# Kernel tuning notes

Hardware: AMD Instinct MI355X
Metric: run time of the kernel (lower is better)

## Reference

```python
import jax, jax.numpy as jnp
import numpy as np

EMB = 768
EPS = 1e-5

def setup_inputs() -> dict:
    key = jax.random.key(0)
    ks = jax.random.split(key, 7)
    B, S, D = 8, 2048, EMB
    s = 1.0 / np.sqrt(D)
    return {
        "h_": jax.random.normal(ks[0], (B, S, D), dtype=jnp.float32),
        "ln_gamma": jnp.ones((D,), jnp.float32),
        "ln_beta": jnp.zeros((D,), jnp.float32),
        "wq": jax.random.normal(ks[1], (D, D), jnp.float32) * s,
        "bq": jax.random.normal(ks[2], (D,), jnp.float32) * 0.01,
        "wk": jax.random.normal(ks[3], (D, D), jnp.float32) * s,
        "bk": jax.random.normal(ks[4], (D,), jnp.float32) * 0.01,
    }

def reference(h_, ln_gamma, ln_beta, wq, bq, wk, bk):
    # LayerNorm over last dim
    mu = jnp.mean(h_, axis=-1, keepdims=True)
    var = jnp.mean(jnp.square(h_ - mu), axis=-1, keepdims=True)
    hn = (h_ - mu) * jax.lax.rsqrt(var + EPS) * ln_gamma + ln_beta
    # Q/K projections (torch Linear: x @ W^T + b; here wq is [D_in, D_out])
    q = jnp.einsum('bsd,de->bse', hn, wq) + bq
    k = jnp.einsum('bsd,de->bse', hn, wk) + bk
    # scores: q @ k^T (no sqrt(d) scaling, matching original)
    w = jnp.einsum('bqd,bkd->bqk', q, k)
    return jax.nn.softmax(w, axis=-1)
```

## Files before the change

kernel.cpp:

```cpp
#include <hip/hip_runtime.h>
#include <stdint.h>

#define EMB   768
#define BATCH 8
#define SEQ   2048
#define ROWS  (BATCH*SEQ)
#define EPS   1e-5f

#define BM 128
#define BN 128
#define BK 32
#define BK2 64

typedef _Float16 half8 __attribute__((ext_vector_type(8)));
typedef _Float16 half4 __attribute__((ext_vector_type(4)));
typedef float    floatx4 __attribute__((ext_vector_type(4)));

__device__ __forceinline__ void g2l16(const void* g, void* l) {
    __builtin_amdgcn_global_load_lds(
        (const __attribute__((address_space(1))) unsigned int*)g,
        (__attribute__((address_space(3))) unsigned int*)l,
        16, 0, 0);
}

__global__ __launch_bounds__(256) void split_w_kernel(
    const float* __restrict__ wq, const float* __restrict__ wk,
    _Float16* __restrict__ wq_hi, _Float16* __restrict__ wq_lo,
    _Float16* __restrict__ wk_hi, _Float16* __restrict__ wk_lo)
{
    const float* src = (blockIdx.y == 0) ? wq : wk;
    _Float16* dh     = (blockIdx.y == 0) ? wq_hi : wk_hi;
    _Float16* dl     = (blockIdx.y == 0) ? wq_lo : wk_lo;
    int i4 = blockIdx.x * 256 + threadIdx.x;
    float4 v = ((const float4*)src)[i4];
    half4 vh, vl;
    float c[4] = {v.x, v.y, v.z, v.w};
#pragma unroll
    for (int t = 0; t < 4; t++) {
        _Float16 hi = (_Float16)c[t];
        vh[t] = hi;
        vl[t] = (_Float16)(c[t] - (float)hi);
    }
    ((half4*)dh)[i4] = vh;
    ((half4*)dl)[i4] = vl;
}

__global__ __launch_bounds__(256) void wtilde_kernel(
    const float* __restrict__ wk, const float* __restrict__ bq,
    float* __restrict__ wt)
{
    int row  = blockIdx.x * 4 + (threadIdx.x >> 6);
    int lane = threadIdx.x & 63;
    const float4* r4 = (const float4*)(wk + (size_t)row * EMB);
    const float4* b4 = (const float4*)bq;
    float s = 0.f;
#pragma unroll
    for (int j = 0; j < 3; j++) {
        float4 a = r4[lane + j * 64];
        float4 b = b4[lane + j * 64];
        s += a.x * b.x + a.y * b.y + a.z * b.z + a.w * b.w;
    }
#pragma unroll
    for (int sh = 1; sh < 64; sh <<= 1) s += __shfl_xor(s, sh, 64);
    if (lane == 0) wt[row] = s;
}

__global__ __launch_bounds__(256) void ln_kernel(
    const float* __restrict__ h,
    const float* __restrict__ gamma,
    const float* __restrict__ beta,
    const float* __restrict__ wt,
    _Float16* __restrict__ hn_hi,
    float* __restrict__ v_out)
{
    int row  = blockIdx.x * 4 + (threadIdx.x >> 6);
    int lane = threadIdx.x & 63;
    const float4* hr4 = (const float4*)(h + (size_t)row * EMB);
    float4 x[3];
    float s1 = 0.f, s2 = 0.f;
#pragma unroll
    for (int j = 0; j < 3; j++) {
        x[j] = hr4[lane + j * 64];
        s1 += x[j].x + x[j].y + x[j].z + x[j].w;
        s2 += x[j].x * x[j].x + x[j].y * x[j].y + x[j].z * x[j].z + x[j].w * x[j].w;
    }
#pragma unroll
    for (int s = 1; s < 64; s <<= 1) {
        s1 += __shfl_xor(s1, s, 64);
        s2 += __shfl_xor(s2, s, 64);
    }
    float mu  = s1 * (1.0f / EMB);
    float var = s2 * (1.0f / EMB) - mu * mu;
    float rs  = rsqrtf(var + EPS);
    _Float16* oh = hn_hi + (size_t)row * EMB;
    float vsum = 0.f;
#pragma unroll
    for (int j = 0; j < 3; j++) {
        int e4 = lane + j * 64;
        float4 g = ((const float4*)gamma)[e4];
        float4 b = ((const float4*)beta)[e4];
        float4 w = ((const float4*)wt)[e4];
        float v[4] = {
            (x[j].x - mu) * rs * g.x + b.x,
            (x[j].y - mu) * rs * g.y + b.y,
            (x[j].z - mu) * rs * g.z + b.z,
            (x[j].w - mu) * rs * g.w + b.w };
        vsum += v[0] * w.x + v[1] * w.y + v[2] * w.z + v[3] * w.w;
        half4 vh;
#pragma unroll
        for (int t = 0; t < 4; t++) vh[t] = (_Float16)v[t];
        *(half4*)(oh + e4 * 4) = vh;
    }
#pragma unroll
    for (int s = 1; s < 64; s <<= 1) vsum += __shfl_xor(vsum, s, 64);
    if (lane == 0) v_out[row] = vsum;
}

__global__ __launch_bounds__(256) void gt_kernel(
    const _Float16* __restrict__ wk_hi, const _Float16* __restrict__ wk_lo,
    const _Float16* __restrict__ wq_hi, const _Float16* __restrict__ wq_lo,
    _Float16* __restrict__ gt_hi, _Float16* __restrict__ gt_lo)
{
    __shared__ __attribute__((aligned(16))) _Float16 Ah_s[BM * BK];
    __shared__ __attribute__((aligned(16))) _Float16 Al_s[BM * BK];
    __shared__ __attribute__((aligned(16))) _Float16 Bh_s[BN * BK];
    __shared__ __attribute__((aligned(16))) _Float16 Bl_s[BN * BK];

    int rowbase = blockIdx.y * BM;
    int colbase = blockIdx.x * BN;
    int tid  = threadIdx.x;
    int lane = tid & 63, wave = tid >> 6;
    int wrow = (wave >> 1) * 64, wcol = (wave & 1) * 64;

    floatx4 acc[4][4];
#pragma unroll
    for (int i = 0; i < 4; i++)
#pragma unroll
        for (int j = 0; j < 4; j++) acc[i][j] = (floatx4){0.f, 0.f, 0.f, 0.f};

    size_t arow = (size_t)(rowbase + tid / 4) * EMB;
    size_t brow = (size_t)(colbase + tid / 4) * EMB;
    int    boff = (((tid % 4) ^ ((tid >> 3) & 3)) * 16);
    const char* gAh = (const char*)(wk_hi + arow) + boff;
    const char* gAl = (const char*)(wk_lo + arow) + boff;
    const char* gBh = (const char*)(wq_hi + brow) + boff;
    const char* gBl = (const char*)(wq_lo + brow) + boff;
    char* lAh = (char*)Ah_s + tid * 16;
    char* lAl = (char*)Al_s + tid * 16;
    char* lBh = (char*)Bh_s + tid * 16;
    char* lBl = (char*)Bl_s + tid * 16;
    const size_t half_stride = (size_t)64 * EMB * 2;

    for (int k0 = 0; k0 < EMB; k0 += BK) {
        __syncthreads();
        g2l16(gAh, lAh); g2l16(gAh + half_stride, lAh + 4096);
        g2l16(gAl, lAl); g2l16(gAl + half_stride, lAl + 4096);
        g2l16(gBh, lBh); g2l16(gBh + half_stride, lBh + 4096);
        g2l16(gBl, lBl); g2l16(gBl + half_stride, lBl + 4096);
        gAh += 64; gAl += 64; gBh += 64; gBl += 64;
        __syncthreads();

        half8 ah[4], al[4], bh[4], bl[4];
#pragma unroll
        for (int i = 0; i < 4; i++) {
            int roff = wrow + i * 16 + (lane & 15);
            int off = roff * 64 + ((((lane >> 4)) ^ ((roff >> 1) & 3)) * 16);
            ah[i] = *(const half8*)((const char*)Ah_s + off);
            al[i] = *(const half8*)((const char*)Al_s + off);
        }
#pragma unroll
        for (int j = 0; j < 4; j++) {
            int coff = wcol + j * 16 + (lane & 15);
            int off = coff * 64 + ((((lane >> 4)) ^ ((coff >> 1) & 3)) * 16);
            bh[j] = *(const half8*)((const char*)Bh_s + off);
            bl[j] = *(const half8*)((const char*)Bl_s + off);
        }
#pragma unroll
        for (int i = 0; i < 4; i++)
#pragma unroll
            for (int j = 0; j < 4; j++) {
                acc[i][j] = __builtin_amdgcn_mfma_f32_16x16x32_f16(ah[i], bh[j], acc[i][j], 0, 0, 0);
                acc[i][j] = __builtin_amdgcn_mfma_f32_16x16x32_f16(ah[i], bl[j], acc[i][j], 0, 0, 0);
                acc[i][j] = __builtin_amdgcn_mfma_f32_16x16x32_f16(al[i], bh[j], acc[i][j], 0, 0, 0);
            }
    }

#pragma unroll
    for (int j = 0; j < 4; j++) {
        int col = colbase + wcol + j * 16 + (lane & 15);
#pragma unroll
        for (int i = 0; i < 4; i++) {
#pragma unroll
            for (int r = 0; r < 4; r++) {
                int row = rowbase + wrow + i * 16 + (lane >> 4) * 4 + r;
                float v = acc[i][j][r];
                _Float16 hi = (_Float16)v;
                gt_hi[(size_t)row * EMB + col] = hi;
                gt_lo[(size_t)row * EMB + col] = (_Float16)(v - (float)hi);
            }
        }
    }
}

__global__ __launch_bounds__(256) void t_kernel(
    const _Float16* __restrict__ hn_hi,
    const _Float16* __restrict__ gt_hi, const _Float16* __restrict__ gt_lo,
    _Float16* __restrict__ t_hi)
{
    __shared__ __attribute__((aligned(16))) _Float16 Ah_s[BM * BK2];
    __shared__ __attribute__((aligned(16))) _Float16 Bh_s[BN * BK2];
    __shared__ __attribute__((aligned(16))) _Float16 Bl_s[BN * BK2];

    int rowbase = blockIdx.y * BM;
    int colbase = blockIdx.x * BN;
    int tid  = threadIdx.x;
    int lane = tid & 63, wave = tid >> 6;
    int wrow = (wave >> 1) * 64, wcol = (wave & 1) * 64;

    floatx4 acc[4][4];
#pragma unroll
    for (int i = 0; i < 4; i++)
#pragma unroll
        for (int j = 0; j < 4; j++) acc[i][j] = (floatx4){0.f, 0.f, 0.f, 0.f};

    size_t arow = (size_t)(rowbase + tid / 8) * EMB;
    size_t brow = (size_t)(colbase + tid / 8) * EMB;
    int    boff = (((tid % 8) ^ ((tid >> 3) & 7)) * 16);
    const char* gAh = (const char*)(hn_hi + arow) + boff;
    const char* gBh = (const char*)(gt_hi + brow) + boff;
    const char* gBl = (const char*)(gt_lo + brow) + boff;
    char* lAh = (char*)Ah_s + tid * 16;
    char* lBh = (char*)Bh_s + tid * 16;
    char* lBl = (char*)Bl_s + tid * 16;
    const size_t pstride = (size_t)32 * EMB * 2;

    for (int k0 = 0; k0 < EMB; k0 += BK2) {
        __syncthreads();
#pragma unroll
        for (int p = 0; p < 4; p++) {
            g2l16(gAh + p * pstride, lAh + p * 4096);
            g2l16(gBh + p * pstride, lBh + p * 4096);
            g2l16(gBl + p * pstride, lBl + p * 4096);
        }
        gAh += 128; gBh += 128; gBl += 128;
        __syncthreads();

#pragma unroll
        for (int ko = 0; ko < 2; ko++) {
            half8 ah[4], bh[4], bl[4];
#pragma unroll
            for (int i = 0; i < 4; i++) {
                int roff = wrow + i * 16 + (lane & 15);
                int off = roff * 128 + ((ko * 64 + (lane >> 4) * 16) ^ ((roff & 7) << 4));
                ah[i] = *(const half8*)((const char*)Ah_s + off);
            }
#pragma unroll
            for (int j = 0; j < 4; j++) {
                int coff = wcol + j * 16 + (lane & 15);
                int off = coff * 128 + ((ko * 64 + (lane >> 4) * 16) ^ ((coff & 7) << 4));
                bh[j] = *(const half8*)((const char*)Bh_s + off);
                bl[j] = *(const half8*)((const char*)Bl_s + off);
            }
#pragma unroll
            for (int i = 0; i < 4; i++)
#pragma unroll
                for (int j = 0; j < 4; j++) {
                    acc[i][j] = __builtin_amdgcn_mfma_f32_16x16x32_f16(ah[i], bh[j], acc[i][j], 0, 0, 0);
                    acc[i][j] = __builtin_amdgcn_mfma_f32_16x16x32_f16(ah[i], bl[j], acc[i][j], 0, 0, 0);
                }
        }
    }

#pragma unroll
    for (int j = 0; j < 4; j++) {
        int col = colbase + wcol + j * 16 + (lane & 15);
#pragma unroll
        for (int i = 0; i < 4; i++) {
#pragma unroll
            for (int r = 0; r < 4; r++) {
                int row = rowbase + wrow + i * 16 + (lane >> 4) * 4 + r;
                t_hi[(size_t)row * EMB + col] = (_Float16)acc[i][j][r];
            }
        }
    }
}

template<bool F16OUT>
__global__ __launch_bounds__(256) void scores_kernel(
    const _Float16* __restrict__ t_hi,
    const _Float16* __restrict__ hn_hi,
    const float* __restrict__ v_in,
    float* __restrict__ out,
    _Float16* __restrict__ pt,
    float2* __restrict__ state)
{
    __shared__ __attribute__((aligned(16))) _Float16 Ah_s[2][BM * BK];
    __shared__ __attribute__((aligned(16))) _Float16 Bh_s[2][BN * BK];
    __shared__ float red[128][2];

    int b = blockIdx.z;
    size_t base = (size_t)b * SEQ * EMB;
    int rowbase = blockIdx.y * BM;
    int colbase = blockIdx.x * BN;
    int tid  = threadIdx.x;
    int lane = tid & 63, wave = tid >> 6;
    int wrow = (wave >> 1) * 64, wcol = (wave & 1) * 64;

    floatx4 acc[4][4];
#pragma unroll
    for (int i = 0; i < 4; i++)
#pragma unroll
        for (int j = 0; j < 4; j++) acc[i][j] = (floatx4){0.f, 0.f, 0.f, 0.f};

    size_t arow = base + (size_t)(rowbase + tid / 4) * EMB;
    size_t brow = base + (size_t)(colbase + tid / 4) * EMB;
    int    boff = (((tid % 4) ^ ((tid >> 3) & 3)) * 16);
    const char* gAh = (const char*)(t_hi + arow) + boff;
    const char* gBh = (const char*)(hn_hi + brow) + boff;
    const size_t half_stride = (size_t)64 * EMB * 2;

    auto STAGE = [&](int c) {
        char* lA = (char*)Ah_s[c] + tid * 16;
        char* lB = (char*)Bh_s[c] + tid * 16;
        g2l16(gAh, lA); g2l16(gAh + half_stride, lA + 4096);
        g2l16(gBh, lB); g2l16(gBh + half_stride, lB + 4096);
        gAh += 64; gBh += 64;
    };

    const int NT = EMB / BK;
    STAGE(0);
#pragma unroll 2
    for (int t = 0; t < NT; t++) {
        int cur = t & 1;
        asm volatile("" ::: "memory");
        if (t < NT - 1) {
            STAGE(cur ^ 1);
            asm volatile("s_waitcnt vmcnt(4)" ::: "memory");
        } else {
            asm volatile("s_waitcnt vmcnt(0)" ::: "memory");
        }
        __builtin_amdgcn_s_barrier();
        asm volatile("" ::: "memory");

        half8 ah[4], bh[4];
#pragma unroll
        for (int i = 0; i < 4; i++) {
            int roff = wrow + i * 16 + (lane & 15);
            int off = roff * 64 + ((((lane >> 4)) ^ ((roff >> 1) & 3)) * 16);
            ah[i] = *(const half8*)((const char*)Ah_s[cur] + off);
        }
#pragma unroll
        for (int j = 0; j < 4; j++) {
            int coff = wcol + j * 16 + (lane & 15);
            int off = coff * 64 + ((((lane >> 4)) ^ ((coff >> 1) & 3)) * 16);
            bh[j] = *(const half8*)((const char*)Bh_s[cur] + off);
        }
#pragma unroll
        for (int i = 0; i < 4; i++)
#pragma unroll
            for (int j = 0; j < 4; j++)
                acc[i][j] = __builtin_amdgcn_mfma_f32_16x16x32_f16(ah[i], bh[j], acc[i][j], 0, 0, 0);
        asm volatile("" ::: "memory");
        __builtin_amdgcn_s_barrier();
    }

    const float* vb = v_in + (size_t)b * SEQ + colbase;
#pragma unroll
    for (int j = 0; j < 4; j++) {
        float vv = vb[wcol + j * 16 + (lane & 15)];
#pragma unroll
        for (int i = 0; i < 4; i++)
#pragma unroll
            for (int r = 0; r < 4; r++) acc[i][j][r] += vv;
    }

    float m1[4][4];
#pragma unroll
    for (int i = 0; i < 4; i++)
#pragma unroll
        for (int r = 0; r < 4; r++) {
            float m = fmaxf(fmaxf(acc[i][0][r], acc[i][1][r]), fmaxf(acc[i][2][r], acc[i][3][r]));
#pragma unroll
            for (int s = 1; s < 16; s <<= 1) m = fmaxf(m, __shfl_xor(m, s, 64));
            m1[i][r] = m;
        }
    if ((lane & 15) == 0) {
#pragma unroll
        for (int i = 0; i < 4; i++)
#pragma unroll
            for (int r = 0; r < 4; r++)
                red[wrow + i * 16 + (lane >> 4) * 4 + r][wave & 1] = m1[i][r];
    }
    __syncthreads();
    float mrow[4][4];
#pragma unroll
    for (int i = 0; i < 4; i++)
#pragma unroll
        for (int r = 0; r < 4; r++) {
            int rr = wrow + i * 16 + (lane >> 4) * 4 + r;
            mrow[i][r] = fmaxf(red[rr][0], red[rr][1]);
        }
    __syncthreads();

    float ls[4][4];
#pragma unroll
    for (int i = 0; i < 4; i++)
#pragma unroll
        for (int r = 0; r < 4; r++) {
            float s = 0.f;
#pragma unroll
            for (int j = 0; j < 4; j++) {
                float e = __expf(acc[i][j][r] - mrow[i][r]);
                acc[i][j][r] = e;
                s += e;
            }
#pragma unroll
            for (int sh = 1; sh < 16; sh <<= 1) s += __shfl_xor(s, sh, 64);
            ls[i][r] = s;
        }
    if ((lane & 15) == 0) {
#pragma unroll
        for (int i = 0; i < 4; i++)
#pragma unroll
            for (int r = 0; r < 4; r++)
                red[wrow + i * 16 + (lane >> 4) * 4 + r][wave & 1] = ls[i][r];
    }
    __syncthreads();

    size_t outbase = (size_t)b * SEQ * SEQ;
#pragma unroll
    for (int i = 0; i < 4; i++)
#pragma unroll
        for (int j = 0; j < 4; j++)
#pragma unroll
            for (int r = 0; r < 4; r++) {
                int row = rowbase + wrow + i * 16 + (lane >> 4) * 4 + r;
                int col = colbase + wcol + j * 16 + (lane & 15);
                if (F16OUT)
                    pt[outbase + (size_t)row * SEQ + col] = (_Float16)acc[i][j][r];
                else
                    out[outbase + (size_t)row * SEQ + col] = acc[i][j][r];
            }

    if ((wave & 1) == 0 && (lane & 15) == 0) {
#pragma unroll
        for (int i = 0; i < 4; i++)
#pragma unroll
            for (int r = 0; r < 4; r++) {
                int rr = wrow + i * 16 + (lane >> 4) * 4 + r;
                float l = red[rr][0] + red[rr][1];
                state[((size_t)b * SEQ + rowbase + rr) * 16 + blockIdx.x] =
                    make_float2(mrow[i][r], l);
            }
    }
}

template<bool F16IN>
__global__ __launch_bounds__(256) void fixup_kernel(
    float* __restrict__ out,
    const _Float16* __restrict__ pt,
    const float2* __restrict__ state)
{
    int row  = blockIdx.x * 4 + (threadIdx.x >> 6);
    int lane = threadIdx.x & 63;
    float2 v = state[(size_t)row * 16 + (lane & 15)];
    float M = v.x;
#pragma unroll
    for (int s = 1; s < 16; s <<= 1) M = fmaxf(M, __shfl_xor(M, s, 64));
    float e  = __expf(v.x - M);
    float Lp = v.y * e;
#pragma unroll
    for (int s = 1; s < 16; s <<= 1) Lp += __shfl_xor(Lp, s, 64);
    float fv = e / Lp;

    if (F16IN) {
        const half8* p8 = (const half8*)(pt + (size_t)row * SEQ);
        float4* o4 = (float4*)(out + (size_t)row * SEQ);
#pragma unroll
        for (int c0 = 0; c0 < 4; c0++) {
            int i8 = c0 * 64 + lane;
            float s = __shfl(fv, i8 >> 4, 64);
            half8 h = p8[i8];
            float4 a, bqv;
            a.x = (float)h[0] * s; a.y = (float)h[1] * s;
            a.z = (float)h[2] * s; a.w = (float)h[3] * s;
            bqv.x = (float)h[4] * s; bqv.y = (float)h[5] * s;
            bqv.z = (float)h[6] * s; bqv.w = (float)h[7] * s;
            o4[i8 * 2]     = a;
            o4[i8 * 2 + 1] = bqv;
        }
    } else {
        float4* o4 = (float4*)(out + (size_t)row * SEQ);
#pragma unroll
        for (int c0 = 0; c0 < 8; c0++) {
            int i4 = c0 * 64 + lane;
            float s = __shfl(fv, i4 >> 5, 64);
            float4 w = o4[i4];
            w.x *= s; w.y *= s; w.z *= s; w.w *= s;
            o4[i4] = w;
        }
    }
}

extern "C" void kernel_launch(void* const* d_in, const int* in_sizes, int n_in,
                              void* d_out, int out_size, void* d_ws, size_t ws_size,
                              hipStream_t stream)
{
    const float* h  = (const float*)d_in[0];
    const float* g  = (const float*)d_in[1];
    const float* be = (const float*)d_in[2];
    const float* wq = (const float*)d_in[3];
    const float* bq = (const float*)d_in[4];
    const float* wk = (const float*)d_in[5];
    const float* bk = (const float*)d_in[6];
    (void)bk;
    float* out = (float*)d_out;

    char* ws = (char*)d_ws;
    const size_t SZ  = (size_t)ROWS * EMB * 2;
    const size_t WSZ = (size_t)EMB * EMB * 2;
    _Float16* hn_hi = (_Float16*)(ws);
    _Float16* t_hi  = (_Float16*)(ws + SZ);
    char* wbase = ws + 2 * SZ;
    _Float16* wq_hi = (_Float16*)(wbase);
    _Float16* wq_lo = (_Float16*)(wbase + WSZ);
    _Float16* wk_hi = (_Float16*)(wbase + 2 * WSZ);
    _Float16* wk_lo = (_Float16*)(wbase + 3 * WSZ);
    _Float16* gt_hi = (_Float16*)(wbase + 4 * WSZ);
    _Float16* gt_lo = (_Float16*)(wbase + 5 * WSZ);
    char* sbase = wbase + 6 * WSZ;
    float*  wt = (float*)(sbase);
    float*  v  = (float*)(sbase + 4096);
    float2* st = (float2*)(sbase + 4096 + 65536);
    char*   ptb = sbase + 4096 + 65536 + (size_t)ROWS * 16 * sizeof(float2);
    const size_t PTSZ = (size_t)BATCH * SEQ * SEQ * 2;
    _Float16* pt = (_Float16*)ptb;
    bool use_f16 = ws_size >= (size_t)(ptb - ws) + PTSZ;

    split_w_kernel<<<dim3(576, 2), 256, 0, stream>>>(wq, wk, wq_hi, wq_lo, wk_hi, wk_lo);
    wtilde_kernel<<<dim3(EMB / 4), 256, 0, stream>>>(wk, bq, wt);
    ln_kernel<<<dim3(ROWS / 4), 256, 0, stream>>>(h, g, be, wt, hn_hi, v);
    gt_kernel<<<dim3(EMB / BN, EMB / BM), 256, 0, stream>>>(wk_hi, wk_lo, wq_hi, wq_lo, gt_hi, gt_lo);
    t_kernel<<<dim3(EMB / BN, ROWS / BM), 256, 0, stream>>>(hn_hi, gt_hi, gt_lo, t_hi);
    if (use_f16) {
        scores_kernel<true><<<dim3(SEQ / BN, SEQ / BM, BATCH), 256, 0, stream>>>(t_hi, hn_hi, v, out, pt, st);
        fixup_kernel<true><<<dim3(ROWS / 4), 256, 0, stream>>>(out, pt, st);
    } else {
        scores_kernel<false><<<dim3(SEQ / BN, SEQ / BM, BATCH), 256, 0, stream>>>(t_hi, hn_hi, v, out, nullptr, st);
        fixup_kernel<false><<<dim3(ROWS / 4), 256, 0, stream>>>(out, nullptr, st);
    }
}
```

Baseline: 381.2 us.

## Enlarge scores kernel tile to 256x256 with 512 threads

The scores GEMM+softmax kernel moves from 128x128 tiles with 4 waves to 256x256 tiles with 8 waves, each wave computing a 128x64 sub-tile with an 8x4 MFMA accumulator array. The larger tile cuts global/L2 traffic per FLOP and halves the number of per-row partial softmax states, so the fixup kernel now merges 8 partials instead of 16. MFMA issue is wrapped in s_setprio. The trade-off is much higher register pressure (128 accumulator floats per lane) and fewer blocks per CU.

```diff
diff --git a/kernel.cpp b/kernel.cpp
--- a/kernel.cpp
+++ b/kernel.cpp
@@ -286,7 +286,7 @@
 }
 
 template<bool F16OUT>
-__global__ __launch_bounds__(256) void scores_kernel(
+__global__ __launch_bounds__(512, 2) void scores_kernel(
     const _Float16* __restrict__ t_hi,
     const _Float16* __restrict__ hn_hi,
     const float* __restrict__ v_in,
@@ -294,47 +294,46 @@
     _Float16* __restrict__ pt,
     float2* __restrict__ state)
 {
-    __shared__ __attribute__((aligned(16))) _Float16 Ah_s[2][BM * BK];
-    __shared__ __attribute__((aligned(16))) _Float16 Bh_s[2][BN * BK];
-    __shared__ float red[128][2];
+    __shared__ __attribute__((aligned(16))) _Float16 Ah_s[2][256 * BK];
+    __shared__ __attribute__((aligned(16))) _Float16 Bh_s[2][256 * BK];
 
     int b = blockIdx.z;
     size_t base = (size_t)b * SEQ * EMB;
-    int rowbase = blockIdx.y * BM;
-    int colbase = blockIdx.x * BN;
+    int rowbase = blockIdx.y * 256;
+    int colbase = blockIdx.x * 256;
     int tid  = threadIdx.x;
     int lane = tid & 63, wave = tid >> 6;
-    int wrow = (wave >> 1) * 64, wcol = (wave & 1) * 64;
-
-    floatx4 acc[4][4];
-#pragma unroll
-    for (int i = 0; i < 4; i++)
-#pragma unroll
-        for (int j = 0; j < 4; j++) acc[i][j] = (floatx4){0.f, 0.f, 0.f, 0.f};
-
-    size_t arow = base + (size_t)(rowbase + tid / 4) * EMB;
-    size_t brow = base + (size_t)(colbase + tid / 4) * EMB;
-    int    boff = (((tid % 4) ^ ((tid >> 3) & 3)) * 16);
-    const char* gAh = (const char*)(t_hi + arow) + boff;
-    const char* gBh = (const char*)(hn_hi + brow) + boff;
-    const size_t half_stride = (size_t)64 * EMB * 2;
-
-    auto STAGE = [&](int c) {
-        char* lA = (char*)Ah_s[c] + tid * 16;
-        char* lB = (char*)Bh_s[c] + tid * 16;
-        g2l16(gAh, lA); g2l16(gAh + half_stride, lA + 4096);
-        g2l16(gBh, lB); g2l16(gBh + half_stride, lB + 4096);
-        gAh += 64; gBh += 64;
+    int wr = wave >> 2, wc = wave & 3;
+    int wrow = wr * 128, wcol = wc * 64;
+
+    floatx4 acc[8][4];
+#pragma unroll
+    for (int m = 0; m < 8; m++)
+#pragma unroll
+        for (int n = 0; n < 4; n++) acc[m][n] = (floatx4){0.f, 0.f, 0.f, 0.f};
+
+    int boff = (((tid & 3) ^ ((tid >> 3) & 3)) * 16);
+    const char* gA0 = (const char*)(t_hi  + base + (size_t)(rowbase + (tid >> 2)) * EMB) + boff;
+    const char* gB0 = (const char*)(hn_hi + base + (size_t)(colbase + (tid >> 2)) * EMB) + boff;
+    const size_t half_stride = (size_t)128 * EMB * 2;
+
+    auto STAGE = [&](int c, int kt) {
+        const char* ga = gA0 + kt * 64;
+        const char* gb = gB0 + kt * 64;
+        char* la = (char*)Ah_s[c] + tid * 16;
+        char* lb = (char*)Bh_s[c] + tid * 16;
+        g2l16(ga, la); g2l16(ga + half_stride, la + 8192);
+        g2l16(gb, lb); g2l16(gb + half_stride, lb + 8192);
     };
 
     const int NT = EMB / BK;
-    STAGE(0);
+    STAGE(0, 0);
 #pragma unroll 2
     for (int t = 0; t < NT; t++) {
         int cur = t & 1;
         asm volatile("" ::: "memory");
         if (t < NT - 1) {
-            STAGE(cur ^ 1);
+            STAGE(cur ^ 1, t + 1);
             asm volatile("s_waitcnt vmcnt(4)" ::: "memory");
         } else {
             asm volatile("s_waitcnt vmcnt(0)" ::: "memory");
@@ -342,115 +341,104 @@
         __builtin_amdgcn_s_barrier();
         asm volatile("" ::: "memory");
 
-        half8 ah[4], bh[4];
-#pragma unroll
-        for (int i = 0; i < 4; i++) {
-            int roff = wrow + i * 16 + (lane & 15);
-            int off = roff * 64 + ((((lane >> 4)) ^ ((roff >> 1) & 3)) * 16);
-            ah[i] = *(const half8*)((const char*)Ah_s[cur] + off);
-        }
-#pragma unroll
-        for (int j = 0; j < 4; j++) {
-            int coff = wcol + j * 16 + (lane & 15);
-            int off = coff * 64 + ((((lane >> 4)) ^ ((coff >> 1) & 3)) * 16);
-            bh[j] = *(const half8*)((const char*)Bh_s[cur] + off);
-        }
-#pragma unroll
-        for (int i = 0; i < 4; i++)
-#pragma unroll
-            for (int j = 0; j < 4; j++)
-                acc[i][j] = __builtin_amdgcn_mfma_f32_16x16x32_f16(ah[i], bh[j], acc[i][j], 0, 0, 0);
+        half8 afr[8], bfr[4];
+        const char* pa = (const char*)Ah_s[cur];
+        const char* pb = (const char*)Bh_s[cur];
+#pragma unroll
+        for (int n = 0; n < 4; n++) {
+            int coff = wcol + n * 16 + (lane & 15);
+            bfr[n] = *(const half8*)(pb + coff * 64 + ((((lane >> 4)) ^ ((coff >> 1) & 3)) * 16));
+        }
+#pragma unroll
+        for (int m = 0; m < 8; m++) {
+            int roff = wrow + m * 16 + (lane & 15);
+            afr[m] = *(const half8*)(pa + roff * 64 + ((((lane >> 4)) ^ ((roff >> 1) & 3)) * 16));
+        }
+        __builtin_amdgcn_s_setprio(1);
+#pragma unroll
+        for (int m = 0; m < 8; m++)
+#pragma unroll
+            for (int n = 0; n < 4; n++)
+                acc[m][n] = __builtin_amdgcn_mfma_f32_16x16x32_f16(afr[m], bfr[n], acc[m][n], 0, 0, 0);
+        __builtin_amdgcn_s_setprio(0);
         asm volatile("" ::: "memory");
         __builtin_amdgcn_s_barrier();
     }
 
+    __syncthreads();
+    float (*red)[4] = (float (*)[4])&Ah_s[0][0];
+
     const float* vb = v_in + (size_t)b * SEQ + colbase;
 #pragma unroll
-    for (int j = 0; j < 4; j++) {
-        float vv = vb[wcol + j * 16 + (lane & 15)];
-#pragma unroll
-        for (int i = 0; i < 4; i++)
-#pragma unroll
-            for (int r = 0; r < 4; r++) acc[i][j][r] += vv;
-    }
-
-    float m1[4][4];
-#pragma unroll
-    for (int i = 0; i < 4; i++)
+    for (int n = 0; n < 4; n++) {
+        float vv = vb[wcol + n * 16 + (lane & 15)];
+#pragma unroll
+        for (int m = 0; m < 8; m++)
+#pragma unroll
+            for (int r = 0; r < 4; r++) acc[m][n][r] += vv;
+    }
+
+#pragma unroll
+    for (int m = 0; m < 8; m++)
 #pragma unroll
         for (int r = 0; r < 4; r++) {
-            float m = fmaxf(fmaxf(acc[i][0][r], acc[i][1][r]), fmaxf(acc[i][2][r], acc[i][3][r]));
-#pragma unroll
-            for (int s = 1; s < 16; s <<= 1) m = fmaxf(m, __shfl_xor(m, s, 64));
-            m1[i][r] = m;
-        }
-    if ((lane & 15) == 0) {
-#pragma unroll
-        for (int i = 0; i < 4; i++)
-#pragma unroll
-            for (int r = 0; r < 4; r++)
-                red[wrow + i * 16 + (lane >> 4) * 4 + r][wave & 1] = m1[i][r];
-    }
+            float mx = fmaxf(fmaxf(acc[m][0][r], acc[m][1][r]), fmaxf(acc[m][2][r], acc[m][3][r]));
+#pragma unroll
+            for (int sh = 1; sh < 16; sh <<= 1) mx = fmaxf(mx, __shfl_xor(mx, sh, 64));
+            if ((lane & 15) == 0) red[wrow + m * 16 + (lane >> 4) * 4 + r][wc] = mx;
+        }
     __syncthreads();
-    float mrow[4][4];
-#pragma unroll
-    for (int i = 0; i < 4; i++)
+    float mrow[8][4];
+#pragma unroll
+    for (int m = 0; m < 8; m++)
 #pragma unroll
         for (int r = 0; r < 4; r++) {
-            int rr = wrow + i * 16 + (lane >> 4) * 4 + r;
-            mrow[i][r] = fmaxf(red[rr][0], red[rr][1]);
+            int row = wrow + m * 16 + (lane >> 4) * 4 + r;
+            mrow[m][r] = fmaxf(fmaxf(red[row][0], red[row][1]), fmaxf(red[row][2], red[row][3]));
         }
     __syncthreads();
 
-    float ls[4][4];
-#pragma unroll
-    for (int i = 0; i < 4; i++)
+#pragma unroll
+    for (int m = 0; m < 8; m++)
 #pragma unroll
         for (int r = 0; r < 4; r++) {
-            float s = 0.f;
-#pragma unroll
-            for (int j = 0; j < 4; j++) {
-                float e = __expf(acc[i][j][r] - mrow[i][r]);
-                acc[i][j][r] = e;
-                s += e;
-            }
-#pragma unroll
-            for (int sh = 1; sh < 16; sh <<= 1) s += __shfl_xor(s, sh, 64);
-            ls[i][r] = s;
-        }
-    if ((lane & 15) == 0) {
-#pragma unroll
-        for (int i = 0; i < 4; i++)
-#pragma unroll
-            for (int r = 0; r < 4; r++)
-                red[wrow + i * 16 + (lane >> 4) * 4 + r][wave & 1] = ls[i][r];
-    }
+            float ssum = 0.f;
+#pragma unroll
+            for (int n = 0; n < 4; n++) {
+                float e = __expf(acc[m][n][r] - mrow[m][r]);
+                acc[m][n][r] = e;
+                ssum += e;
+            }
+#pragma unroll
+            for (int sh = 1; sh < 16; sh <<= 1) ssum += __shfl_xor(ssum, sh, 64);
+            if ((lane & 15) == 0) red[wrow + m * 16 + (lane >> 4) * 4 + r][wc] = ssum;
+        }
     __syncthreads();
 
     size_t outbase = (size_t)b * SEQ * SEQ;
 #pragma unroll
-    for (int i = 0; i < 4; i++)
-#pragma unroll
-        for (int j = 0; j < 4; j++)
+    for (int m = 0; m < 8; m++)
+#pragma unroll
+        for (int n = 0; n < 4; n++)
 #pragma unroll
             for (int r = 0; r < 4; r++) {
-                int row = rowbase + wrow + i * 16 + (lane >> 4) * 4 + r;
-                int col = colbase + wcol + j * 16 + (lane & 15);
+                int row = rowbase + wrow + m * 16 + (lane >> 4) * 4 + r;
+                int col = colbase + wcol + n * 16 + (lane & 15);
                 if (F16OUT)
-                    pt[outbase + (size_t)row * SEQ + col] = (_Float16)acc[i][j][r];
+                    pt[outbase + (size_t)row * SEQ + col] = (_Float16)acc[m][n][r];
                 else
-                    out[outbase + (size_t)row * SEQ + col] = acc[i][j][r];
-            }
-
-    if ((wave & 1) == 0 && (lane & 15) == 0) {
-#pragma unroll
-        for (int i = 0; i < 4; i++)
+                    out[outbase + (size_t)row * SEQ + col] = acc[m][n][r];
+            }
+
+    if (wc == 0 && (lane & 15) == 0) {
+#pragma unroll
+        for (int m = 0; m < 8; m++)
 #pragma unroll
             for (int r = 0; r < 4; r++) {
-                int rr = wrow + i * 16 + (lane >> 4) * 4 + r;
-                float l = red[rr][0] + red[rr][1];
-                state[((size_t)b * SEQ + rowbase + rr) * 16 + blockIdx.x] =
-                    make_float2(mrow[i][r], l);
+                int rr = wrow + m * 16 + (lane >> 4) * 4 + r;
+                float l = red[rr][0] + red[rr][1] + red[rr][2] + red[rr][3];
+                state[((size_t)b * SEQ + rowbase + rr) * 8 + blockIdx.x] =
+                    make_float2(mrow[m][r], l);
             }
     }
 }
@@ -463,14 +451,14 @@
 {
     int row  = blockIdx.x * 4 + (threadIdx.x >> 6);
     int lane = threadIdx.x & 63;
-    float2 v = state[(size_t)row * 16 + (lane & 15)];
+    float2 v = state[(size_t)row * 8 + (lane & 7)];
     float M = v.x;
 #pragma unroll
-    for (int s = 1; s < 16; s <<= 1) M = fmaxf(M, __shfl_xor(M, s, 64));
+    for (int s = 1; s < 8; s <<= 1) M = fmaxf(M, __shfl_xor(M, s, 64));
     float e  = __expf(v.x - M);
     float Lp = v.y * e;
 #pragma unroll
-    for (int s = 1; s < 16; s <<= 1) Lp += __shfl_xor(Lp, s, 64);
+    for (int s = 1; s < 8; s <<= 1) Lp += __shfl_xor(Lp, s, 64);
     float fv = e / Lp;
 
     if (F16IN) {
@@ -479,7 +467,7 @@
 #pragma unroll
         for (int c0 = 0; c0 < 4; c0++) {
             int i8 = c0 * 64 + lane;
-            float s = __shfl(fv, i8 >> 4, 64);
+            float s = __shfl(fv, i8 >> 5, 64);
             half8 h = p8[i8];
             float4 a, bqv;
             a.x = (float)h[0] * s; a.y = (float)h[1] * s;
@@ -494,7 +482,7 @@
 #pragma unroll
         for (int c0 = 0; c0 < 8; c0++) {
             int i4 = c0 * 64 + lane;
-            float s = __shfl(fv, i4 >> 5, 64);
+            float s = __shfl(fv, i4 >> 6, 64);
             float4 w = o4[i4];
             w.x *= s; w.y *= s; w.z *= s; w.w *= s;
             o4[i4] = w;
@@ -543,10 +531,10 @@
     gt_kernel<<<dim3(EMB / BN, EMB / BM), 256, 0, stream>>>(wk_hi, wk_lo, wq_hi, wq_lo, gt_hi, gt_lo);
     t_kernel<<<dim3(EMB / BN, ROWS / BM), 256, 0, stream>>>(hn_hi, gt_hi, gt_lo, t_hi);
     if (use_f16) {
-        scores_kernel<true><<<dim3(SEQ / BN, SEQ / BM, BATCH), 256, 0, stream>>>(t_hi, hn_hi, v, out, pt, st);
+        scores_kernel<true><<<dim3(SEQ / 256, SEQ / 256, BATCH), 512, 0, stream>>>(t_hi, hn_hi, v, out, pt, st);
         fixup_kernel<true><<<dim3(ROWS / 4), 256, 0, stream>>>(out, pt, st);
     } else {
-        scores_kernel<false><<<dim3(SEQ / BN, SEQ / BM, BATCH), 256, 0, stream>>>(t_hi, hn_hi, v, out, nullptr, st);
+        scores_kernel<false><<<dim3(SEQ / 256, SEQ / 256, BATCH), 512, 0, stream>>>(t_hi, hn_hi, v, out, nullptr, st);
         fixup_kernel<false><<<dim3(ROWS / 4), 256, 0, stream>>>(out, nullptr, st);
     }
 }
```

Result: no change. 381.9 us (+0.2%).

## Shrink gt tiles, deepen scores K-step to 64, and swizzle block order

Applied to the files above, without the earlier changes.

The gt_kernel now uses 64x64 tiles, giving 144 blocks instead of 36 so the small weight-product GEMM fills more compute units. The scores kernel stages 64-wide K slices per pipeline step with a new 8-way XOR swizzle, halving the number of barriers and iterations. It also remaps block IDs so that consecutive launched blocks are spread across batches and tiles, which changes cache locality. The costs are double the LDS per block in scores (lower occupancy) and more global-to-LDS loads in flight per stage.

```diff
diff --git a/kernel.cpp b/kernel.cpp
--- a/kernel.cpp
+++ b/kernel.cpp
@@ -121,26 +121,26 @@
     const _Float16* __restrict__ wq_hi, const _Float16* __restrict__ wq_lo,
     _Float16* __restrict__ gt_hi, _Float16* __restrict__ gt_lo)
 {
-    __shared__ __attribute__((aligned(16))) _Float16 Ah_s[BM * BK];
-    __shared__ __attribute__((aligned(16))) _Float16 Al_s[BM * BK];
-    __shared__ __attribute__((aligned(16))) _Float16 Bh_s[BN * BK];
-    __shared__ __attribute__((aligned(16))) _Float16 Bl_s[BN * BK];
-
-    int rowbase = blockIdx.y * BM;
-    int colbase = blockIdx.x * BN;
+    __shared__ __attribute__((aligned(16))) _Float16 Ah_s[64 * BK];
+    __shared__ __attribute__((aligned(16))) _Float16 Al_s[64 * BK];
+    __shared__ __attribute__((aligned(16))) _Float16 Bh_s[64 * BK];
+    __shared__ __attribute__((aligned(16))) _Float16 Bl_s[64 * BK];
+
+    int rowbase = blockIdx.y * 64;
+    int colbase = blockIdx.x * 64;
     int tid  = threadIdx.x;
     int lane = tid & 63, wave = tid >> 6;
-    int wrow = (wave >> 1) * 64, wcol = (wave & 1) * 64;
-
-    floatx4 acc[4][4];
-#pragma unroll
-    for (int i = 0; i < 4; i++)
-#pragma unroll
-        for (int j = 0; j < 4; j++) acc[i][j] = (floatx4){0.f, 0.f, 0.f, 0.f};
-
-    size_t arow = (size_t)(rowbase + tid / 4) * EMB;
-    size_t brow = (size_t)(colbase + tid / 4) * EMB;
-    int    boff = (((tid % 4) ^ ((tid >> 3) & 3)) * 16);
+    int wrow = (wave >> 1) * 32, wcol = (wave & 1) * 32;
+
+    floatx4 acc[2][2];
+#pragma unroll
+    for (int i = 0; i < 2; i++)
+#pragma unroll
+        for (int j = 0; j < 2; j++) acc[i][j] = (floatx4){0.f, 0.f, 0.f, 0.f};
+
+    size_t arow = (size_t)(rowbase + (tid >> 2)) * EMB;
+    size_t brow = (size_t)(colbase + (tid >> 2)) * EMB;
+    int    boff = (((tid & 3) ^ ((tid >> 3) & 3)) * 16);
     const char* gAh = (const char*)(wk_hi + arow) + boff;
     const char* gAl = (const char*)(wk_lo + arow) + boff;
     const char* gBh = (const char*)(wq_hi + brow) + boff;
@@ -149,36 +149,33 @@
     char* lAl = (char*)Al_s + tid * 16;
     char* lBh = (char*)Bh_s + tid * 16;
     char* lBl = (char*)Bl_s + tid * 16;
-    const size_t half_stride = (size_t)64 * EMB * 2;
 
     for (int k0 = 0; k0 < EMB; k0 += BK) {
         __syncthreads();
-        g2l16(gAh, lAh); g2l16(gAh + half_stride, lAh + 4096);
-        g2l16(gAl, lAl); g2l16(gAl + half_stride, lAl + 4096);
-        g2l16(gBh, lBh); g2l16(gBh + half_stride, lBh + 4096);
-        g2l16(gBl, lBl); g2l16(gBl + half_stride, lBl + 4096);
+        g2l16(gAh, lAh); g2l16(gAl, lAl);
+        g2l16(gBh, lBh); g2l16(gBl, lBl);
         gAh += 64; gAl += 64; gBh += 64; gBl += 64;
         __syncthreads();
 
-        half8 ah[4], al[4], bh[4], bl[4];
-#pragma unroll
-        for (int i = 0; i < 4; i++) {
+        half8 ah[2], al[2], bh[2], bl[2];
+#pragma unroll
+        for (int i = 0; i < 2; i++) {
             int roff = wrow + i * 16 + (lane & 15);
             int off = roff * 64 + ((((lane >> 4)) ^ ((roff >> 1) & 3)) * 16);
             ah[i] = *(const half8*)((const char*)Ah_s + off);
             al[i] = *(const half8*)((const char*)Al_s + off);
         }
 #pragma unroll
-        for (int j = 0; j < 4; j++) {
+        for (int j = 0; j < 2; j++) {
             int coff = wcol + j * 16 + (lane & 15);
             int off = coff * 64 + ((((lane >> 4)) ^ ((coff >> 1) & 3)) * 16);
             bh[j] = *(const half8*)((const char*)Bh_s + off);
             bl[j] = *(const half8*)((const char*)Bl_s + off);
         }
 #pragma unroll
-        for (int i = 0; i < 4; i++)
-#pragma unroll
-            for (int j = 0; j < 4; j++) {
+        for (int i = 0; i < 2; i++)
+#pragma unroll
+            for (int j = 0; j < 2; j++) {
                 acc[i][j] = __builtin_amdgcn_mfma_f32_16x16x32_f16(ah[i], bh[j], acc[i][j], 0, 0, 0);
                 acc[i][j] = __builtin_amdgcn_mfma_f32_16x16x32_f16(ah[i], bl[j], acc[i][j], 0, 0, 0);
                 acc[i][j] = __builtin_amdgcn_mfma_f32_16x16x32_f16(al[i], bh[j], acc[i][j], 0, 0, 0);
@@ -186,10 +183,10 @@
     }
 
 #pragma unroll
-    for (int j = 0; j < 4; j++) {
+    for (int j = 0; j < 2; j++) {
         int col = colbase + wcol + j * 16 + (lane & 15);
 #pragma unroll
-        for (int i = 0; i < 4; i++) {
+        for (int i = 0; i < 2; i++) {
 #pragma unroll
             for (int r = 0; r < 4; r++) {
                 int row = rowbase + wrow + i * 16 + (lane >> 4) * 4 + r;
@@ -294,14 +291,19 @@
     _Float16* __restrict__ pt,
     float2* __restrict__ state)
 {
-    __shared__ __attribute__((aligned(16))) _Float16 Ah_s[2][BM * BK];
-    __shared__ __attribute__((aligned(16))) _Float16 Bh_s[2][BN * BK];
+    __shared__ __attribute__((aligned(16))) _Float16 Ah_s[2][BM * BK2];
+    __shared__ __attribute__((aligned(16))) _Float16 Bh_s[2][BN * BK2];
     __shared__ float red[128][2];
 
-    int b = blockIdx.z;
+    int id  = ((int)blockIdx.z << 8) | ((int)blockIdx.y << 4) | (int)blockIdx.x;
+    int vid = (id & 7) * 256 + (id >> 3);
+    int b   = vid >> 8;
+    int by  = (vid >> 4) & 15;
+    int bx  = vid & 15;
+
     size_t base = (size_t)b * SEQ * EMB;
-    int rowbase = blockIdx.y * BM;
-    int colbase = blockIdx.x * BN;
+    int rowbase = by * BM;
+    int colbase = bx * BN;
     int tid  = threadIdx.x;
     int lane = tid & 63, wave = tid >> 6;
     int wrow = (wave >> 1) * 64, wcol = (wave & 1) * 64;
@@ -312,22 +314,29 @@
 #pragma unroll
         for (int j = 0; j < 4; j++) acc[i][j] = (floatx4){0.f, 0.f, 0.f, 0.f};
 
-    size_t arow = base + (size_t)(rowbase + tid / 4) * EMB;
-    size_t brow = base + (size_t)(colbase + tid / 4) * EMB;
-    int    boff = (((tid % 4) ^ ((tid >> 3) & 3)) * 16);
+    size_t arow = base + (size_t)(rowbase + tid / 8) * EMB;
+    size_t brow = base + (size_t)(colbase + tid / 8) * EMB;
+    int    boff = (((tid % 8) ^ ((tid >> 3) & 7)) * 16);
     const char* gAh = (const char*)(t_hi + arow) + boff;
     const char* gBh = (const char*)(hn_hi + brow) + boff;
-    const size_t half_stride = (size_t)64 * EMB * 2;
+    char* lAh0 = (char*)Ah_s[0] + tid * 16;
+    char* lBh0 = (char*)Bh_s[0] + tid * 16;
+    char* lAh1 = (char*)Ah_s[1] + tid * 16;
+    char* lBh1 = (char*)Bh_s[1] + tid * 16;
+    const size_t pstride = (size_t)32 * EMB * 2;
 
     auto STAGE = [&](int c) {
-        char* lA = (char*)Ah_s[c] + tid * 16;
-        char* lB = (char*)Bh_s[c] + tid * 16;
-        g2l16(gAh, lA); g2l16(gAh + half_stride, lA + 4096);
-        g2l16(gBh, lB); g2l16(gBh + half_stride, lB + 4096);
-        gAh += 64; gBh += 64;
+        char* lA = c ? lAh1 : lAh0;
+        char* lB = c ? lBh1 : lBh0;
+#pragma unroll
+        for (int p = 0; p < 4; p++) {
+            g2l16(gAh + p * pstride, lA + p * 4096);
+            g2l16(gBh + p * pstride, lB + p * 4096);
+        }
+        gAh += 128; gBh += 128;
     };
 
-    const int NT = EMB / BK;
+    const int NT = EMB / BK2;
     STAGE(0);
 #pragma unroll 2
     for (int t = 0; t < NT; t++) {
@@ -335,31 +344,34 @@
         asm volatile("" ::: "memory");
         if (t < NT - 1) {
             STAGE(cur ^ 1);
-            asm volatile("s_waitcnt vmcnt(4)" ::: "memory");
+            asm volatile("s_waitcnt vmcnt(8)" ::: "memory");
         } else {
             asm volatile("s_waitcnt vmcnt(0)" ::: "memory");
         }
         __builtin_amdgcn_s_barrier();
         asm volatile("" ::: "memory");
 
-        half8 ah[4], bh[4];
-#pragma unroll
-        for (int i = 0; i < 4; i++) {
-            int roff = wrow + i * 16 + (lane & 15);
-            int off = roff * 64 + ((((lane >> 4)) ^ ((roff >> 1) & 3)) * 16);
-            ah[i] = *(const half8*)((const char*)Ah_s[cur] + off);
-        }
-#pragma unroll
-        for (int j = 0; j < 4; j++) {
-            int coff = wcol + j * 16 + (lane & 15);
-            int off = coff * 64 + ((((lane >> 4)) ^ ((coff >> 1) & 3)) * 16);
-            bh[j] = *(const half8*)((const char*)Bh_s[cur] + off);
-        }
-#pragma unroll
-        for (int i = 0; i < 4; i++)
-#pragma unroll
-            for (int j = 0; j < 4; j++)
-                acc[i][j] = __builtin_amdgcn_mfma_f32_16x16x32_f16(ah[i], bh[j], acc[i][j], 0, 0, 0);
+#pragma unroll
+        for (int ko = 0; ko < 2; ko++) {
+            half8 ah[4], bh[4];
+#pragma unroll
+            for (int i = 0; i < 4; i++) {
+                int roff = wrow + i * 16 + (lane & 15);
+                int off = roff * 128 + ((ko * 64 + (lane >> 4) * 16) ^ ((roff & 7) << 4));
+                ah[i] = *(const half8*)((const char*)Ah_s[cur] + off);
+            }
+#pragma unroll
+            for (int j = 0; j < 4; j++) {
+                int coff = wcol + j * 16 + (lane & 15);
+                int off = coff * 128 + ((ko * 64 + (lane >> 4) * 16) ^ ((coff & 7) << 4));
+                bh[j] = *(const half8*)((const char*)Bh_s[cur] + off);
+            }
+#pragma unroll
+            for (int i = 0; i < 4; i++)
+#pragma unroll
+                for (int j = 0; j < 4; j++)
+                    acc[i][j] = __builtin_amdgcn_mfma_f32_16x16x32_f16(ah[i], bh[j], acc[i][j], 0, 0, 0);
+        }
         asm volatile("" ::: "memory");
         __builtin_amdgcn_s_barrier();
     }
@@ -449,7 +461,7 @@
             for (int r = 0; r < 4; r++) {
                 int rr = wrow + i * 16 + (lane >> 4) * 4 + r;
                 float l = red[rr][0] + red[rr][1];
-                state[((size_t)b * SEQ + rowbase + rr) * 16 + blockIdx.x] =
+                state[((size_t)b * SEQ + rowbase + rr) * 16 + bx] =
                     make_float2(mrow[i][r], l);
             }
     }
@@ -540,7 +552,7 @@
     split_w_kernel<<<dim3(576, 2), 256, 0, stream>>>(wq, wk, wq_hi, wq_lo, wk_hi, wk_lo);
     wtilde_kernel<<<dim3(EMB / 4), 256, 0, stream>>>(wk, bq, wt);
     ln_kernel<<<dim3(ROWS / 4), 256, 0, stream>>>(h, g, be, wt, hn_hi, v);
-    gt_kernel<<<dim3(EMB / BN, EMB / BM), 256, 0, stream>>>(wk_hi, wk_lo, wq_hi, wq_lo, gt_hi, gt_lo);
+    gt_kernel<<<dim3(EMB / 64, EMB / 64), 256, 0, stream>>>(wk_hi, wk_lo, wq_hi, wq_lo, gt_hi, gt_lo);
     t_kernel<<<dim3(EMB / BN, ROWS / BM), 256, 0, stream>>>(hn_hi, gt_hi, gt_lo, t_hi);
     if (use_f16) {
         scores_kernel<true><<<dim3(SEQ / BN, SEQ / BM, BATCH), 256, 0, stream>>>(t_hi, hn_hi, v, out, pt, st);
```

Result: faster. 354.1 us (-7.1%).
